# Optimization experiments

Measured on AMD Instinct MI355X. Metric: run time of the kernel, lower is better.

## Reference

```python
import jax, jax.numpy as jnp
import numpy as np

INPUT_SIZE = 64
HIDDEN = 128


def setup_inputs() -> dict:
    key = jax.random.key(0)
    ks = jax.random.split(key, 10)
    B, T, I, H = 512, 1024, INPUT_SIZE, HIDDEN
    s_ih = 1.0 / np.sqrt(H)
    inp = {
        "x": jax.random.normal(ks[0], (B, T, I), dtype=jnp.float32),
        # PyTorch nn.LSTM params, gate order (i, f, g, o)
        "W_ih": jax.random.uniform(ks[1], (4 * H, I), jnp.float32, -s_ih, s_ih),
        "W_hh": jax.random.uniform(ks[2], (4 * H, H), jnp.float32, -s_ih, s_ih),
        "b_ih": jax.random.uniform(ks[3], (4 * H,), jnp.float32, -s_ih, s_ih),
        "b_hh": jax.random.uniform(ks[4], (4 * H,), jnp.float32, -s_ih, s_ih),
        # fc1: 128 -> 256, fc2: 256 -> 1 (PyTorch Linear init bounds)
        "W1": jax.random.uniform(ks[5], (256, H), jnp.float32, -s_ih, s_ih),
        "b1": jax.random.uniform(ks[6], (256,), jnp.float32, -s_ih, s_ih),
        "W2": jax.random.uniform(ks[7], (1, 256), jnp.float32, -1.0 / 16, 1.0 / 16),
        "b2": jax.random.uniform(ks[8], (1,), jnp.float32, -1.0 / 16, 1.0 / 16),
    }
    return inp


def _lstm_last_hidden(x, W_ih, W_hh, b_ih, b_hh):
    B, T, I = x.shape
    H = W_hh.shape[1]
    # Precompute input projection for all timesteps in one big GEMM: [T, B, 4H]
    x_proj = jnp.einsum("bti,gi->tbg", x, W_ih) + (b_ih + b_hh)

    def step(carry, xp_t):
        h, c = carry
        gates = xp_t + h @ W_hh.T  # [B, 4H]
        i_g, f_g, g_g, o_g = jnp.split(gates, 4, axis=-1)
        i_g = jax.nn.sigmoid(i_g)
        f_g = jax.nn.sigmoid(f_g)
        g_g = jnp.tanh(g_g)
        o_g = jax.nn.sigmoid(o_g)
        c = f_g * c + i_g * g_g
        h = o_g * jnp.tanh(c)
        return (h, c), None

    h0 = jnp.zeros((B, H), dtype=x.dtype)
    c0 = jnp.zeros((B, H), dtype=x.dtype)
    (h_T, _), _ = jax.lax.scan(step, (h0, c0), x_proj)
    return h_T  # [B, H], equals output at last timestep


def reference(x, W_ih, W_hh, b_ih, b_hh, W1, b1, W2, b2):
    h_last = _lstm_last_hidden(x, W_ih, W_hh, b_ih, b_hh)  # x[:, -1, :] of LSTM outputs
    y = h_last @ W1.T + b1   # fc1 (no activation in original)
    y = y @ W2.T + b2        # fc2 -> [B, 1]
    return y
```

## Files before the change

kernel.cpp:

```cpp
#include <hip/hip_runtime.h>


#define T_STEPS 1024
#define ISZ 64
#define HSZ 128
#define ZSZ (ISZ + HSZ)
#define G4 512
#define BCHUNK 2
#define NTH 1024
#define CLEN 24
#define NGATE 4

__device__ __forceinline__ float fast_sigmoid(float x) {
    return 1.0f / (1.0f + __expf(-x));
}

__device__ __forceinline__ float fast_tanh(float x) {
    float xc = fminf(fmaxf(x, -15.0f), 15.0f);
    float u = __expf(2.0f * xc);
    return (u - 1.0f) / (u + 1.0f);
}

__device__ __forceinline__ float dpp_xor1(float v) {
    return __int_as_float(__builtin_amdgcn_mov_dpp(__float_as_int(v), 0xB1, 0xF, 0xF, true));
}
__device__ __forceinline__ float dpp_xor2(float v) {
    return __int_as_float(__builtin_amdgcn_mov_dpp(__float_as_int(v), 0x4E, 0xF, 0xF, true));
}
__device__ __forceinline__ float swz_xor4(float v) {
    return __int_as_float(__builtin_amdgcn_ds_swizzle(__float_as_int(v), 0x101F));
}

__global__ __launch_bounds__(NTH, 4)
void lstm_fused_kernel(const float* __restrict__ x,
                       const float* __restrict__ W_ih,
                       const float* __restrict__ W_hh,
                       const float* __restrict__ b_ih,
                       const float* __restrict__ b_hh,
                       const float* __restrict__ W1,
                       const float* __restrict__ b1,
                       const float* __restrict__ W2,
                       const float* __restrict__ b2,
                       float* __restrict__ out)
{
    __shared__ __align__(16) float zbuf[BCHUNK][ZSZ];
    __shared__ __align__(16) float gbuf[BCHUNK][G4];
    __shared__ float red[BCHUNK][4];

    const int tid = threadIdx.x;
    const int b0 = blockIdx.x * BCHUNK;
    const int c  = tid & 7;
    const int qg = tid >> 3;

    const int g_own = 4 * qg + (c & 3);
    const bool hi4 = (c & 4) != 0;
    const bool hi2 = (c & 2) != 0;
    const bool hi1 = (c & 1) != 0;

    float wt[NGATE][CLEN];
    #pragma unroll
    for (int i = 0; i < NGATE; ++i) {
        const float* rih = W_ih + (size_t)(4 * qg + i) * ISZ;
        const float* rhh = W_hh + (size_t)(4 * qg + i) * HSZ;
        #pragma unroll
        for (int k = 0; k < CLEN; ++k) {
            const int col = c * CLEN + k;
            wt[i][k] = (col < ISZ) ? rih[col] : rhh[col - ISZ];
        }
    }
    const float bias = b_ih[g_own] + b_hh[g_own];

    if (tid < BCHUNK * HSZ) zbuf[tid >> 7][ISZ + (tid & 127)] = 0.0f;
    if (tid >= 256 && tid < 256 + BCHUNK * ISZ) {
        int l = tid - 256;
        zbuf[l >> 6][l & 63] =
            x[((size_t)(b0 + (l >> 6)) * T_STEPS + 0) * ISZ + (l & 63)];
    }
    float cst = 0.0f;
    __syncthreads();

    const int gsel = tid >> 8;

    for (int t = 0; t < T_STEPS; ++t) {
        float xpre = 0.0f;
        const bool pf = (tid >= 512) && (tid < 640) && (t + 1 < T_STEPS);
        if (pf) {
            int l = tid - 512;
            xpre = x[((size_t)(b0 + (l >> 6)) * T_STEPS + (t + 1)) * ISZ + (l & 63)];
        }

        float a[NGATE][2];
        #pragma unroll
        for (int i = 0; i < NGATE; ++i) { a[i][0] = 0.0f; a[i][1] = 0.0f; }
        #pragma unroll
        for (int r = 0; r < BCHUNK; ++r) {
            const float4* zr = reinterpret_cast<const float4*>(zbuf[r]) + c * (CLEN / 4);
            #pragma unroll
            for (int k = 0; k < CLEN / 4; ++k) {
                float4 u = zr[k];
                #pragma unroll
                for (int i = 0; i < NGATE; ++i) {
                    a[i][r] = fmaf(wt[i][4*k  ], u.x, a[i][r]);
                    a[i][r] = fmaf(wt[i][4*k+1], u.y, a[i][r]);
                    a[i][r] = fmaf(wt[i][4*k+2], u.z, a[i][r]);
                    a[i][r] = fmaf(wt[i][4*k+3], u.w, a[i][r]);
                }
            }
        }

        float g4[NGATE];
        #pragma unroll
        for (int i = 0; i < NGATE; ++i) {
            float keep = hi4 ? a[i][1] : a[i][0];
            float send = hi4 ? a[i][0] : a[i][1];
            g4[i] = keep + swz_xor4(send);
        }
        float g2[2];
        {
            float k0 = hi2 ? g4[2] : g4[0];
            float s0 = hi2 ? g4[0] : g4[2];
            float k1 = hi2 ? g4[3] : g4[1];
            float s1 = hi2 ? g4[1] : g4[3];
            g2[0] = k0 + dpp_xor2(s0);
            g2[1] = k1 + dpp_xor2(s1);
        }
        float s;
        {
            float kc = hi1 ? g2[1] : g2[0];
            float sc = hi1 ? g2[0] : g2[1];
            s = kc + dpp_xor1(sc);
        }
        s += bias;

        float v = (gsel == 2) ? fast_tanh(s) : fast_sigmoid(s);
        gbuf[c >> 2][g_own] = v;
        __syncthreads();

        if (tid < BCHUNK * HSZ) {
            const int r = tid >> 7;
            const int j = tid & 127;
            float ig = gbuf[r][j];
            float fg = gbuf[r][j + 128];
            float gv = gbuf[r][j + 256];
            float og = gbuf[r][j + 384];
            cst = fmaf(fg, cst, ig * gv);
            zbuf[r][ISZ + j] = og * fast_tanh(cst);
        } else if (pf) {
            int l = tid - 512;
            zbuf[l >> 6][l & 63] = xpre;
        }
        __syncthreads();
    }

    if (tid < 512) {
        const int b = tid >> 8;
        const int m = tid & 255;
        const float4* w1r = reinterpret_cast<const float4*>(W1 + (size_t)m * HSZ);
        const float4* hr = reinterpret_cast<const float4*>(zbuf[b] + ISZ);
        float acc = 0.0f;
        #pragma unroll
        for (int k = 0; k < HSZ / 4; ++k) {
            float4 w = w1r[k];
            float4 h = hr[k];
            acc = fmaf(w.x, h.x, acc);
            acc = fmaf(w.y, h.y, acc);
            acc = fmaf(w.z, h.z, acc);
            acc = fmaf(w.w, h.w, acc);
        }
        float z = (acc + b1[m]) * W2[m];
        #pragma unroll
        for (int off = 32; off >= 1; off >>= 1)
            z += __shfl_down(z, off, 64);
        if ((tid & 63) == 0) red[b][(tid >> 6) & 3] = z;
    }
    __syncthreads();
    if (tid == 0)   out[b0]     = red[0][0] + red[0][1] + red[0][2] + red[0][3] + b2[0];
    if (tid == 256) out[b0 + 1] = red[1][0] + red[1][1] + red[1][2] + red[1][3] + b2[0];
}

extern "C" void kernel_launch(void* const* d_in, const int* in_sizes, int n_in,
                              void* d_out, int out_size, void* d_ws, size_t ws_size,
                              hipStream_t stream) {
    const float* x    = (const float*)d_in[0];
    const float* W_ih = (const float*)d_in[1];
    const float* W_hh = (const float*)d_in[2];
    const float* b_ih = (const float*)d_in[3];
    const float* b_hh = (const float*)d_in[4];
    const float* W1   = (const float*)d_in[5];
    const float* b1   = (const float*)d_in[6];
    const float* W2   = (const float*)d_in[7];
    const float* b2   = (const float*)d_in[8];
    float* out = (float*)d_out;

    lstm_fused_kernel<<<dim3(512 / BCHUNK), dim3(NTH), 0, stream>>>(
        x, W_ih, W_hh, b_ih, b_hh, W1, b1, W2, b2, out);
}
```

Before: 1.583 ms.

## Remap gates per hidden unit and double-buffer state to drop a barrier

Each group of 8 lanes now owns all four gates of one hidden unit instead of four consecutive gate rows. A full butterfly reduction leaves every lane with the complete gate pre-activations, so the cell and hidden update happen in registers without the shared gate buffer. The z buffer is double-buffered, which removes one of the two block-wide barriers per timestep. In exchange, every thread evaluates five transcendentals and the cell update is computed redundantly across lanes.

```diff
diff --git a/kernel.cpp b/kernel.cpp
--- a/kernel.cpp
+++ b/kernel.cpp
@@ -5,7 +5,6 @@
 #define ISZ 64
 #define HSZ 128
 #define ZSZ (ISZ + HSZ)
-#define G4 512
 #define BCHUNK 2
 #define NTH 1024
 #define CLEN 24
@@ -43,45 +42,44 @@
                        const float* __restrict__ b2,
                        float* __restrict__ out)
 {
-    __shared__ __align__(16) float zbuf[BCHUNK][ZSZ];
-    __shared__ __align__(16) float gbuf[BCHUNK][G4];
+    __shared__ __align__(16) float zbuf[2][BCHUNK][ZSZ];
     __shared__ float red[BCHUNK][4];
 
     const int tid = threadIdx.x;
     const int b0 = blockIdx.x * BCHUNK;
     const int c  = tid & 7;
-    const int qg = tid >> 3;
-
-    const int g_own = 4 * qg + (c & 3);
+    const int j  = tid >> 3;
+    const int myrow = c >> 2;
     const bool hi4 = (c & 4) != 0;
-    const bool hi2 = (c & 2) != 0;
-    const bool hi1 = (c & 1) != 0;
 
     float wt[NGATE][CLEN];
+    float bs[NGATE];
     #pragma unroll
     for (int i = 0; i < NGATE; ++i) {
-        const float* rih = W_ih + (size_t)(4 * qg + i) * ISZ;
-        const float* rhh = W_hh + (size_t)(4 * qg + i) * HSZ;
+        const int g = j + HSZ * i;
+        const float* rih = W_ih + (size_t)g * ISZ;
+        const float* rhh = W_hh + (size_t)g * HSZ;
         #pragma unroll
         for (int k = 0; k < CLEN; ++k) {
             const int col = c * CLEN + k;
             wt[i][k] = (col < ISZ) ? rih[col] : rhh[col - ISZ];
         }
+        bs[i] = b_ih[g] + b_hh[g];
     }
-    const float bias = b_ih[g_own] + b_hh[g_own];
 
-    if (tid < BCHUNK * HSZ) zbuf[tid >> 7][ISZ + (tid & 127)] = 0.0f;
+    if (tid < BCHUNK * HSZ) zbuf[0][tid >> 7][ISZ + (tid & 127)] = 0.0f;
     if (tid >= 256 && tid < 256 + BCHUNK * ISZ) {
         int l = tid - 256;
-        zbuf[l >> 6][l & 63] =
+        zbuf[0][l >> 6][l & 63] =
             x[((size_t)(b0 + (l >> 6)) * T_STEPS + 0) * ISZ + (l & 63)];
     }
     float cst = 0.0f;
     __syncthreads();
 
-    const int gsel = tid >> 8;
+    for (int t = 0; t < T_STEPS; ++t) {
+        const int p = t & 1;
+        const int q = p ^ 1;
 
-    for (int t = 0; t < T_STEPS; ++t) {
         float xpre = 0.0f;
         const bool pf = (tid >= 512) && (tid < 640) && (t + 1 < T_STEPS);
         if (pf) {
@@ -89,12 +87,12 @@
             xpre = x[((size_t)(b0 + (l >> 6)) * T_STEPS + (t + 1)) * ISZ + (l & 63)];
         }
 
-        float a[NGATE][2];
+        float a[NGATE][BCHUNK];
         #pragma unroll
         for (int i = 0; i < NGATE; ++i) { a[i][0] = 0.0f; a[i][1] = 0.0f; }
         #pragma unroll
         for (int r = 0; r < BCHUNK; ++r) {
-            const float4* zr = reinterpret_cast<const float4*>(zbuf[r]) + c * (CLEN / 4);
+            const float4* zr = reinterpret_cast<const float4*>(zbuf[p][r]) + c * (CLEN / 4);
             #pragma unroll
             for (int k = 0; k < CLEN / 4; ++k) {
                 float4 u = zr[k];
@@ -108,46 +106,30 @@
             }
         }
 
-        float g4[NGATE];
-        #pragma unroll
-        for (int i = 0; i < NGATE; ++i) {
-            float keep = hi4 ? a[i][1] : a[i][0];
-            float send = hi4 ? a[i][0] : a[i][1];
-            g4[i] = keep + swz_xor4(send);
+        float s0, s1, s2, s3;
+        {
+            float g0 = (hi4 ? a[0][1] : a[0][0]) + swz_xor4(hi4 ? a[0][0] : a[0][1]);
+            float g1 = (hi4 ? a[1][1] : a[1][0]) + swz_xor4(hi4 ? a[1][0] : a[1][1]);
+            float g2 = (hi4 ? a[2][1] : a[2][0]) + swz_xor4(hi4 ? a[2][0] : a[2][1]);
+            float g3 = (hi4 ? a[3][1] : a[3][0]) + swz_xor4(hi4 ? a[3][0] : a[3][1]);
+            g0 += dpp_xor2(g0); g1 += dpp_xor2(g1); g2 += dpp_xor2(g2); g3 += dpp_xor2(g3);
+            s0 = g0 + dpp_xor1(g0) + bs[0];
+            s1 = g1 + dpp_xor1(g1) + bs[1];
+            s2 = g2 + dpp_xor1(g2) + bs[2];
+            s3 = g3 + dpp_xor1(g3) + bs[3];
         }
-        float g2[2];
-        {
-            float k0 = hi2 ? g4[2] : g4[0];
-            float s0 = hi2 ? g4[0] : g4[2];
-            float k1 = hi2 ? g4[3] : g4[1];
-            float s1 = hi2 ? g4[1] : g4[3];
-            g2[0] = k0 + dpp_xor2(s0);
-            g2[1] = k1 + dpp_xor2(s1);
-        }
-        float s;
-        {
-            float kc = hi1 ? g2[1] : g2[0];
-            float sc = hi1 ? g2[0] : g2[1];
-            s = kc + dpp_xor1(sc);
-        }
-        s += bias;
 
-        float v = (gsel == 2) ? fast_tanh(s) : fast_sigmoid(s);
-        gbuf[c >> 2][g_own] = v;
-        __syncthreads();
+        float ig = fast_sigmoid(s0);
+        float fg = fast_sigmoid(s1);
+        float gv = fast_tanh(s2);
+        float og = fast_sigmoid(s3);
+        cst = fmaf(fg, cst, ig * gv);
+        float hval = og * fast_tanh(cst);
+        if ((c & 3) == 0) zbuf[q][myrow][ISZ + j] = hval;
 
-        if (tid < BCHUNK * HSZ) {
-            const int r = tid >> 7;
-            const int j = tid & 127;
-            float ig = gbuf[r][j];
-            float fg = gbuf[r][j + 128];
-            float gv = gbuf[r][j + 256];
-            float og = gbuf[r][j + 384];
-            cst = fmaf(fg, cst, ig * gv);
-            zbuf[r][ISZ + j] = og * fast_tanh(cst);
-        } else if (pf) {
+        if (pf) {
             int l = tid - 512;
-            zbuf[l >> 6][l & 63] = xpre;
+            zbuf[q][l >> 6][l & 63] = xpre;
         }
         __syncthreads();
     }
@@ -156,7 +138,7 @@
         const int b = tid >> 8;
         const int m = tid & 255;
         const float4* w1r = reinterpret_cast<const float4*>(W1 + (size_t)m * HSZ);
-        const float4* hr = reinterpret_cast<const float4*>(zbuf[b] + ISZ);
+        const float4* hr = reinterpret_cast<const float4*>(zbuf[0][b] + ISZ);
         float acc = 0.0f;
         #pragma unroll
         for (int k = 0; k < HSZ / 4; ++k) {
```

Result: slower. 1.817 ms (+14.7%).
